# Performance work log

Measured on AMD Instinct MI355X. Metric: run time of the kernel, lower is better.

## Reference

```python
import jax, jax.numpy as jnp
import numpy as np

WZ, WH, WW = 2, 6, 12
N = WZ * WH * WW            # 144 tokens per window
DIM, HEADS = 384, 12
HD = DIM // HEADS           # 32
TOW = (8 // WZ) * (48 // WH)  # type_of_windows = 32
NW = 96 // WW               # longitude windows = 8
B_ = 1 * TOW * NW           # 256
TABLE = (2 * WW - 1) * WH * WH * WZ * WZ  # 3312


def _position_index():
    zi = np.arange(WZ); zj = -np.arange(WZ) * WZ
    hi = np.arange(WH); hj = -np.arange(WH) * WH
    w = np.arange(WW)
    c1 = np.stack(np.meshgrid(zi, hi, w, indexing='ij')).reshape(3, -1)
    c2 = np.stack(np.meshgrid(zj, hj, w, indexing='ij')).reshape(3, -1)
    coords = (c1[:, :, None] - c2[:, None, :]).transpose(1, 2, 0)  # (N, N, 3)
    coords[:, :, 2] += WW - 1
    coords[:, :, 1] *= 2 * WW - 1
    coords[:, :, 0] *= (2 * WW - 1) * WH * WH
    return coords.sum(-1).reshape(-1).astype(np.int32)  # (N*N,)


def setup_inputs() -> dict:
    key = jax.random.key(0)
    ks = jax.random.split(key, 7)
    x = jax.random.normal(ks[0], (B_, N, DIM), dtype=jnp.float32)
    mask = jax.random.normal(ks[1], (NW, N, N), dtype=jnp.float32)
    w_qkv = jax.random.normal(ks[2], (DIM, 3 * DIM), dtype=jnp.float32) * 0.02
    b_qkv = jax.random.normal(ks[3], (3 * DIM,), dtype=jnp.float32) * 0.02
    w_out = jax.random.normal(ks[4], (DIM, DIM), dtype=jnp.float32) * 0.02
    b_out = jax.random.normal(ks[5], (DIM,), dtype=jnp.float32) * 0.02
    bias_table = jax.random.normal(ks[6], (TABLE, TOW, HEADS), dtype=jnp.float32) * 0.02
    position_index = jnp.asarray(_position_index())
    return {"x": x, "mask": mask, "w_qkv": w_qkv, "b_qkv": b_qkv,
            "w_out": w_out, "b_out": b_out, "bias_table": bias_table,
            "position_index": position_index}


def reference(x, mask, w_qkv, b_qkv, w_out, b_out, bias_table, position_index):
    Bw, n, C = x.shape
    scale = HD ** -0.5
    qkv = (x @ w_qkv + b_qkv).reshape(Bw, n, 3, HEADS, HD)
    qkv = jnp.transpose(qkv, (2, 0, 3, 1, 4))  # (3, Bw, H, N, hd)
    q, k, v = qkv[0] * scale, qkv[1], qkv[2]
    attn = jnp.einsum('bhnd,bhmd->bhnm', q, k)  # (Bw, H, N, N)
    # Earth-specific bias: gather table rows by position index, tiled per window group
    r = Bw // TOW
    bias = bias_table[jnp.tile(position_index, r)]          # (r*N*N, TOW, H)
    bias = bias.reshape(n, n, -1, HEADS)                    # (N, N, Bw, H)
    bias = jnp.transpose(bias, (2, 3, 0, 1))                # (Bw, H, N, N)
    attn = attn + bias
    nW = mask.shape[0]
    attn = attn.reshape(Bw // nW, nW, HEADS, n, n) + mask[None, :, None]
    attn = jax.nn.softmax(attn.reshape(Bw, HEADS, n, n), axis=-1)
    out = jnp.einsum('bhnm,bhmd->bhnd', attn, v)            # (Bw, H, N, hd)
    out = jnp.transpose(out, (0, 2, 1, 3)).reshape(Bw, n, C)
    return out @ w_out + b_out
```

## Files before the change

### kernel.cpp

```cpp
#include <hip/hip_runtime.h>
#include <hip/hip_fp16.h>
#include <cstdint>
#include <cstddef>

#define NQQ  (144*144)
#define SCALE 0.17677669529663687f

#define AOH   0ull
#define X16H  0ull
#define QH    14155776ull
#define KH    28311552ull
#define VH    42467328ull
#define WTH   56623104ull
#define WOTH  57065472ull
#define MASKH 57212928ull
#define BIASH 57378816ull
#define WS_NEED_BYTES ((BIASH + 3072ull * 2592ull) * 2ull)

typedef _Float16 half8  __attribute__((ext_vector_type(8)));
typedef _Float16 half4v __attribute__((ext_vector_type(4)));
typedef float    f32x4  __attribute__((ext_vector_type(4)));

__launch_bounds__(256)
__global__ void k_prep(const float* __restrict__ X, _Float16* __restrict__ X16,
                       const float* __restrict__ Wq, _Float16* __restrict__ WqT,
                       const float* __restrict__ Wo, _Float16* __restrict__ WoT,
                       const float* __restrict__ M, _Float16* __restrict__ M16,
                       const float* __restrict__ table, const int* __restrict__ pidx,
                       _Float16* __restrict__ biasOut) {
    __shared__ __align__(16) char psm[13888];
    const int bid = blockIdx.x;
    const int t   = threadIdx.x;
    if (bid < 13824) {
        size_t i = (size_t)bid * 256 + t;
        float4 f = *(const float4*)&X[i * 4];
        _Float16 h[4] = {(_Float16)f.x, (_Float16)f.y, (_Float16)f.z, (_Float16)f.w};
        *(ushort4*)&X16[i * 4] = *(ushort4*)h;
        return;
    }
    if (bid >= 14130) {
        _Float16 (*sTb)[18] = (_Float16(*)[18])psm;
        int* rowsL = (int*)(psm + 13824);
        const int j      = bid - 14130;
        const int s_tile = j / 162;
        const int chunk  = j - s_tile * 162;
        const int i0     = chunk * 16;
        if (t < 16) rowsL[t] = pidx[8 * (i0 + t) + s_tile];
        __syncthreads();
#pragma unroll
        for (int rr = 0; rr < 16; ++rr) {
            int row = rowsL[rr];
            sTb[t][rr] = (_Float16)table[(size_t)row * 384 + t];
            if (t < 128) sTb[t + 256][rr] = (_Float16)table[(size_t)row * 384 + t + 256];
        }
        __syncthreads();
        unsigned int* ob = (unsigned int*)biasOut;
#pragma unroll
        for (int v = t; v < 3072; v += 256) {
            int i1h = v >> 3, dw = v & 7;
            ob[(size_t)(s_tile * 384 + i1h) * 1296 + chunk * 8 + dw] =
                *(const unsigned int*)&sTb[i1h][dw * 2];
        }
        return;
    }
    if (bid >= 13968) {
        size_t i = (size_t)(bid - 13968) * 256 + t;
        float4 f = *(const float4*)&M[i * 4];
        _Float16 h[4] = {(_Float16)f.x, (_Float16)f.y, (_Float16)f.z, (_Float16)f.w};
        *(ushort4*)&M16[i * 4] = *(ushort4*)h;
        return;
    }
    _Float16 (*sT)[72] = (_Float16(*)[72])psm;
    const float* W; _Float16* WT; int K, Cn, cb, kb;
    if (bid < 13932) {
        int j = bid - 13824;
        W = Wq; WT = WqT; K = 384; Cn = 1152;
        cb = (j % 18) * 64; kb = (j / 18) * 64;
    } else {
        int j = bid - 13932;
        W = Wo; WT = WoT; K = 384; Cn = 384;
        cb = (j % 6) * 64; kb = (j / 6) * 64;
    }
#pragma unroll
    for (int i = 0; i < 16; ++i) {
        int id = t + 256 * i;
        int kl = id >> 6, cl = id & 63;
        sT[cl][kl] = (_Float16)W[(size_t)(kb + kl) * Cn + cb + cl];
    }
    __syncthreads();
#pragma unroll
    for (int i = 0; i < 16; ++i) {
        int id = t + 256 * i;
        int cl = id >> 6, kl = id & 63;
        WT[(size_t)(cb + cl) * K + kb + kl] = sT[cl][kl];
    }
}

__launch_bounds__(256)
__global__ void k_qkv_gemm_mfma(const _Float16* __restrict__ X16,
                                const _Float16* __restrict__ WT,
                                const float* __restrict__ bq,
                                _Float16* __restrict__ ws16) {
    __shared__ _Float16 sA[128][40];
    __shared__ _Float16 sBT[128][40];
    const int t    = threadIdx.x;
    const int lane = t & 63;
    const int w    = t >> 6;
    const int quad = lane >> 4;
    const int l15  = lane & 15;
    const int r0   = blockIdx.x * 128, c0 = blockIdx.y * 128;
    const int wr   = (w >> 1) * 64, wc = (w & 1) * 64;

    f32x4 acc[4][4] = {};

    for (int kk = 0; kk < 384; kk += 32) {
#pragma unroll
        for (int i = 0; i < 2; ++i) {
            int id  = t + 256 * i;
            int row = id >> 2;
            int ko  = (id & 3) * 8;
            *(uint4*)&sA[row][ko]  = *(const uint4*)&X16[(size_t)(r0 + row) * 384 + kk + ko];
            *(uint4*)&sBT[row][ko] = *(const uint4*)&WT[(size_t)(c0 + row) * 384 + kk + ko];
        }
        __syncthreads();
        half8 a[4], b[4];
#pragma unroll
        for (int i = 0; i < 4; ++i) a[i] = *(const half8*)&sA[wr + 16 * i + l15][quad * 8];
#pragma unroll
        for (int j = 0; j < 4; ++j) b[j] = *(const half8*)&sBT[wc + 16 * j + l15][quad * 8];
#pragma unroll
        for (int i = 0; i < 4; ++i)
#pragma unroll
            for (int j = 0; j < 4; ++j)
                acc[i][j] = __builtin_amdgcn_mfma_f32_16x16x32_f16(a[i], b[j], acc[i][j], 0, 0, 0);
        __syncthreads();
    }

#pragma unroll
    for (int j = 0; j < 4; ++j) {
        int c  = c0 + wc + 16 * j + l15;
        int p  = c / 384;
        int hh = (c >> 5) % 12;
        int d0 = c & 31;
        float bias = bq[c];
        float sc   = (p == 0) ? SCALE : 1.0f;
        size_t base = (p == 0) ? QH : ((p == 1) ? KH : VH);
#pragma unroll
        for (int i = 0; i < 4; ++i) {
#pragma unroll
            for (int reg = 0; reg < 4; ++reg) {
                int r  = r0 + wr + 16 * i + quad * 4 + reg;
                int bw = r / 144;
                int n  = r - bw * 144;
                ws16[base + (((size_t)bw * 12 + hh) * 144 + n) * 32 + d0] =
                    (_Float16)((acc[i][j][reg] + bias) * sc);
            }
        }
    }
}

__launch_bounds__(576)
__global__ void k_attn_fused_mfma(const _Float16* __restrict__ ws16,
                                  const _Float16* __restrict__ mask16,
                                  const float* __restrict__ table,
                                  const int* __restrict__ pidx,
                                  const _Float16* __restrict__ bias_pre,
                                  _Float16* __restrict__ AO) {
    __shared__ __align__(16) char smem[27616];
    _Float16 (*sK)[40]   = (_Float16(*)[40])(smem);
    _Float16 (*sVT)[168] = (_Float16(*)[168])(smem + 11520);
    _Float16* sBias      = (_Float16*)(smem + 22272);

    const int bh = blockIdx.x;
    const int b  = bh / 12;
    const int h  = bh - b * 12;
    const int t  = threadIdx.x;
    const int w    = t >> 6;
    const int lane = t & 63;
    const int quad = lane >> 4;
    const int l15  = lane & 15;

    const int s_tile = b >> 5;
    const int i1     = b & 31;

    const _Float16* qg = ws16 + QH + (size_t)bh * 4608;
    const _Float16* kg = ws16 + KH + (size_t)bh * 4608;
    const _Float16* vg = ws16 + VH + (size_t)bh * 4608;

    half8 aq = *(const half8*)&qg[(size_t)(16 * w + l15) * 32 + quad * 8];

    {
        int row = t >> 2, ko = (t & 3) * 8;
        *(uint4*)&sK[row][ko] = *(const uint4*)&kg[row * 32 + ko];
    }
    for (int i = t; i < 2304; i += 576) {
        unsigned int u = ((const unsigned int*)vg)[i];
        int m  = i >> 4, d0 = (i & 15) * 2;
        int mp = m ^ ((d0 >> 3) << 3);
        sVT[d0][mp]     = ((const _Float16*)&u)[0];
        sVT[d0 + 1][mp] = ((const _Float16*)&u)[1];
    }
    if (t < 512) {
        int d = t & 31, m = 144 + (t >> 5);
        sVT[d][m ^ ((d >> 3) << 3)] = (_Float16)0;
    }
    if (bias_pre) {
        const _Float16* bg = bias_pre + (size_t)bh * 2592;
        for (int i2 = t; i2 < 648; i2 += 576) {
            uint2 wv = *(const uint2*)&bg[i2 * 4];
            int r18 = i2 / 36;
            int col = i2 * 4 - r18 * 144;
            *(uint2*)&sBias[r18 * 148 + col] = wv;
        }
    } else {
        for (int i = t; i < 2592; i += 576) {
            int row = pidx[8 * i + s_tile];
            int r18 = i / 144;
            sBias[r18 * 148 + (i - r18 * 144)] =
                (_Float16)table[(size_t)row * 384 + i1 * 12 + h];
        }
    }
    __syncthreads();

    f32x4 tj[9] = {};
#pragma unroll
    for (int j = 0; j < 9; ++j) {
        half8 bk = *(const half8*)&sK[16 * j + l15][quad * 8];
        tj[j] = __builtin_amdgcn_mfma_f32_16x16x32_f16(bk, aq, tj[j], 0, 0, 0);
    }

    const int q    = 16 * w + l15;
    const int nb18 = q % 18;
    const _Float16* mrow = mask16 + (size_t)(b & 7) * NQQ + (size_t)q * 144 + 4 * quad;
    uint2 mz[9];
#pragma unroll
    for (int j = 0; j < 9; ++j) mz[j] = *(const uint2*)&mrow[16 * j];
#pragma unroll
    for (int j = 0; j < 9; ++j) {
        uint2 bz = *(const uint2*)&sBias[nb18 * 148 + 16 * j + 4 * quad];
        const _Float16* bb = (const _Float16*)&bz;
        const _Float16* mm = (const _Float16*)&mz[j];
#pragma unroll
        for (int reg = 0; reg < 4; ++reg)
            tj[j][reg] += (float)bb[reg] + (float)mm[reg];
    }
    float rmax = tj[0][0];
#pragma unroll
    for (int j = 0; j < 9; ++j)
#pragma unroll
        for (int reg = 0; reg < 4; ++reg) rmax = fmaxf(rmax, tj[j][reg]);
    rmax = fmaxf(rmax, __shfl_xor(rmax, 16));
    rmax = fmaxf(rmax, __shfl_xor(rmax, 32));
    float rsum = 0.0f;
#pragma unroll
    for (int j = 0; j < 9; ++j)
#pragma unroll
        for (int reg = 0; reg < 4; ++reg) {
            tj[j][reg] = __expf(tj[j][reg] - rmax);
            rsum += tj[j][reg];
        }
    rsum += __shfl_xor(rsum, 16);
    rsum += __shfl_xor(rsum, 32);
    const float inv = 1.0f / rsum;

    unsigned int pkA[10], pkB[10];
    pkA[9] = 0u; pkB[9] = 0u;
#pragma unroll
    for (int j = 0; j < 9; ++j) {
        auto a2 = __builtin_amdgcn_cvt_pkrtz(tj[j][0] * inv, tj[j][1] * inv);
        auto b2 = __builtin_amdgcn_cvt_pkrtz(tj[j][2] * inv, tj[j][3] * inv);
        pkA[j] = *(unsigned int*)&a2;
        pkB[j] = *(unsigned int*)&b2;
    }

    const int src_lo = 32 * (quad & 1) + l15;
    const int src_hi = src_lo + 16;
    const bool selhi = (quad >> 1) != 0;
    f32x4 o[2] = {};
#pragma unroll
    for (int kt = 0; kt < 5; ++kt) {
        const int j0 = 2 * kt, j1 = 2 * kt + 1;
        unsigned int a0l = __shfl((int)pkA[j0], src_lo);
        unsigned int a1l = __shfl((int)pkA[j1], src_lo);
        unsigned int b0l = __shfl((int)pkB[j0], src_lo);
        unsigned int b1l = __shfl((int)pkB[j1], src_lo);
        unsigned int a0h = __shfl((int)pkA[j0], src_hi);
        unsigned int a1h = __shfl((int)pkA[j1], src_hi);
        unsigned int b0h = __shfl((int)pkB[j0], src_hi);
        unsigned int b1h = __shfl((int)pkB[j1], src_hi);
        union { uint4 u4; half8 h8; } bp;
        bp.u4.x = selhi ? a1l : a0l;
        bp.u4.y = selhi ? b1l : b0l;
        bp.u4.z = selhi ? a1h : a0h;
        bp.u4.w = selhi ? b1h : b0h;
#pragma unroll
        for (int dt = 0; dt < 2; ++dt) {
            const int vrow = dt * 16 + l15;
            half8 av = *(const half8*)&sVT[vrow][(kt * 32 + quad * 8) ^ ((vrow >> 3) << 3)];
            o[dt] = __builtin_amdgcn_mfma_f32_16x16x32_f16(av, bp.h8, o[dt], 0, 0, 0);
        }
    }

#pragma unroll
    for (int dt = 0; dt < 2; ++dt) {
        int d = dt * 16 + quad * 4;
        half4v hv;
#pragma unroll
        for (int reg = 0; reg < 4; ++reg) hv[reg] = (_Float16)o[dt][reg];
        *(half4v*)&AO[((size_t)b * 144 + q) * 384 + h * 32 + d] = hv;
    }
}

__launch_bounds__(256)
__global__ void k_out_gemm_mfma(const _Float16* __restrict__ A16,
                                const _Float16* __restrict__ WoT,
                                const float* __restrict__ bo,
                                float* __restrict__ out) {
    __shared__ _Float16 sA[128][40];
    __shared__ _Float16 sBT[128][40];
    const int t    = threadIdx.x;
    const int lane = t & 63;
    const int w    = t >> 6;
    const int quad = lane >> 4;
    const int l15  = lane & 15;
    const int r0   = blockIdx.x * 128, c0 = blockIdx.y * 128;
    const int wr   = (w >> 1) * 64, wc = (w & 1) * 64;

    f32x4 acc[4][4] = {};

    for (int kk = 0; kk < 384; kk += 32) {
#pragma unroll
        for (int i = 0; i < 2; ++i) {
            int id  = t + 256 * i;
            int row = id >> 2;
            int ko  = (id & 3) * 8;
            *(uint4*)&sA[row][ko]  = *(const uint4*)&A16[(size_t)(r0 + row) * 384 + kk + ko];
            *(uint4*)&sBT[row][ko] = *(const uint4*)&WoT[(size_t)(c0 + row) * 384 + kk + ko];
        }
        __syncthreads();
        half8 a[4], b[4];
#pragma unroll
        for (int i = 0; i < 4; ++i) a[i] = *(const half8*)&sA[wr + 16 * i + l15][quad * 8];
#pragma unroll
        for (int j = 0; j < 4; ++j) b[j] = *(const half8*)&sBT[wc + 16 * j + l15][quad * 8];
#pragma unroll
        for (int i = 0; i < 4; ++i)
#pragma unroll
            for (int j = 0; j < 4; ++j)
                acc[i][j] = __builtin_amdgcn_mfma_f32_16x16x32_f16(a[i], b[j], acc[i][j], 0, 0, 0);
        __syncthreads();
    }

#pragma unroll
    for (int j = 0; j < 4; ++j) {
        int c = c0 + wc + 16 * j + l15;
        float bias = bo[c];
#pragma unroll
        for (int i = 0; i < 4; ++i) {
#pragma unroll
            for (int reg = 0; reg < 4; ++reg) {
                int r = r0 + wr + 16 * i + quad * 4 + reg;
                out[(size_t)r * 384 + c] = acc[i][j][reg] + bias;
            }
        }
    }
}

extern "C" void kernel_launch(void* const* d_in, const int* in_sizes, int n_in,
                              void* d_out, int out_size, void* d_ws, size_t ws_size,
                              hipStream_t stream) {
    const float* x      = (const float*)d_in[0];
    const float* mask   = (const float*)d_in[1];
    const float* w_qkv  = (const float*)d_in[2];
    const float* b_qkv  = (const float*)d_in[3];
    const float* w_out  = (const float*)d_in[4];
    const float* b_out  = (const float*)d_in[5];
    const float* table  = (const float*)d_in[6];
    const int*   pidx   = (const int*)d_in[7];
    float* out = (float*)d_out;
    _Float16* ws16 = (_Float16*)d_ws;

    const bool pre = ws_size >= (size_t)WS_NEED_BYTES;
    _Float16* bias16 = pre ? (ws16 + BIASH) : (_Float16*)nullptr;

    hipLaunchKernelGGL(k_prep,          dim3(pre ? 15426 : 14130), dim3(256), 0, stream,
                       x, ws16 + X16H, w_qkv, ws16 + WTH, w_out, ws16 + WOTH,
                       mask, ws16 + MASKH, table, pidx, bias16);
    hipLaunchKernelGGL(k_qkv_gemm_mfma, dim3(288, 9), dim3(256), 0, stream,
                       ws16 + X16H, ws16 + WTH, b_qkv, ws16);
    hipLaunchKernelGGL(k_attn_fused_mfma, dim3(3072), dim3(576), 0, stream,
                       ws16, ws16 + MASKH, table, pidx, bias16, ws16 + AOH);
    hipLaunchKernelGGL(k_out_gemm_mfma, dim3(288, 3), dim3(256), 0, stream,
                       ws16 + AOH, ws16 + WOTH, b_out, out);
}
```

Measured before the change: 287.2 us.

## Use direct global-to-LDS loads, XOR swizzle and XCD-aware block remap in GEMMs

Both MFMA GEMM kernels now stage tiles with global_load_lds, which writes directly from global memory into LDS without passing through registers. The K step grows from 32 to 64, and an XOR-swizzled LDS layout is used so the half8 fragment reads avoid bank conflicts. Launches become 1D with a block-index remap that groups tiles across the 8 XCDs for better L2 locality. This roughly halves the barrier count per tile and cuts register traffic, at the cost of more LDS per block and reliance on the swizzle being consistent between the writes and the reads.

```diff
diff --git a/kernel.cpp b/kernel.cpp
--- a/kernel.cpp
+++ b/kernel.cpp
@@ -20,6 +20,10 @@
 typedef _Float16 half8  __attribute__((ext_vector_type(8)));
 typedef _Float16 half4v __attribute__((ext_vector_type(4)));
 typedef float    f32x4  __attribute__((ext_vector_type(4)));
+
+typedef __attribute__((address_space(1))) const unsigned int guint;
+typedef __attribute__((address_space(3))) unsigned int luint;
+#define GLD16(g, l) __builtin_amdgcn_global_load_lds((guint*)(g), (luint*)(l), 16, 0, 0)
 
 __launch_bounds__(256)
 __global__ void k_prep(const float* __restrict__ X, _Float16* __restrict__ X16,
@@ -101,38 +105,53 @@
                                 const _Float16* __restrict__ WT,
                                 const float* __restrict__ bq,
                                 _Float16* __restrict__ ws16) {
-    __shared__ _Float16 sA[128][40];
-    __shared__ _Float16 sBT[128][40];
+    __shared__ __align__(16) _Float16 sA[128 * 64];
+    __shared__ __align__(16) _Float16 sB[128 * 64];
     const int t    = threadIdx.x;
     const int lane = t & 63;
     const int w    = t >> 6;
     const int quad = lane >> 4;
     const int l15  = lane & 15;
-    const int r0   = blockIdx.x * 128, c0 = blockIdx.y * 128;
-    const int wr   = (w >> 1) * 64, wc = (w & 1) * 64;
+    const int bid = blockIdx.x;
+    const int wg  = (bid & 7) * 324 + (bid >> 3);
+    const int cy  = wg % 9, rx = wg / 9;
+    const int r0  = rx * 128, c0 = cy * 128;
+    const int wr  = (w >> 1) * 64, wc = (w & 1) * 64;
+
+    const int drow = t >> 3;
+    const int schk = (t & 7) ^ (drow & 7);
+    const _Float16* gA = &X16[(size_t)(r0 + drow) * 384 + schk * 8];
+    const _Float16* gB = &WT [(size_t)(c0 + drow) * 384 + schk * 8];
+    char* lA = (char*)sA + t * 16;
+    char* lB = (char*)sB + t * 16;
+
+    const int x7 = l15 & 7;
+    const char* rA = (const char*)sA + (wr + l15) * 128;
+    const char* rB = (const char*)sB + (wc + l15) * 128;
 
     f32x4 acc[4][4] = {};
 
-    for (int kk = 0; kk < 384; kk += 32) {
-#pragma unroll
-        for (int i = 0; i < 2; ++i) {
-            int id  = t + 256 * i;
-            int row = id >> 2;
-            int ko  = (id & 3) * 8;
-            *(uint4*)&sA[row][ko]  = *(const uint4*)&X16[(size_t)(r0 + row) * 384 + kk + ko];
-            *(uint4*)&sBT[row][ko] = *(const uint4*)&WT[(size_t)(c0 + row) * 384 + kk + ko];
-        }
-        __syncthreads();
-        half8 a[4], b[4];
-#pragma unroll
-        for (int i = 0; i < 4; ++i) a[i] = *(const half8*)&sA[wr + 16 * i + l15][quad * 8];
-#pragma unroll
-        for (int j = 0; j < 4; ++j) b[j] = *(const half8*)&sBT[wc + 16 * j + l15][quad * 8];
-#pragma unroll
-        for (int i = 0; i < 4; ++i)
-#pragma unroll
-            for (int j = 0; j < 4; ++j)
-                acc[i][j] = __builtin_amdgcn_mfma_f32_16x16x32_f16(a[i], b[j], acc[i][j], 0, 0, 0);
+    for (int kk = 0; kk < 384; kk += 64) {
+#pragma unroll
+        for (int j = 0; j < 4; ++j) {
+            GLD16(gA + (size_t)j * 12288 + kk, lA + j * 4096);
+            GLD16(gB + (size_t)j * 12288 + kk, lB + j * 4096);
+        }
+        __syncthreads();
+#pragma unroll
+        for (int s = 0; s < 2; ++s) {
+            const int ca = (((s * 4 + quad) ^ x7) << 4);
+            half8 a[4], b[4];
+#pragma unroll
+            for (int i = 0; i < 4; ++i) a[i] = *(const half8*)(rA + i * 2048 + ca);
+#pragma unroll
+            for (int j = 0; j < 4; ++j) b[j] = *(const half8*)(rB + j * 2048 + ca);
+#pragma unroll
+            for (int i = 0; i < 4; ++i)
+#pragma unroll
+                for (int j = 0; j < 4; ++j)
+                    acc[i][j] = __builtin_amdgcn_mfma_f32_16x16x32_f16(a[i], b[j], acc[i][j], 0, 0, 0);
+        }
         __syncthreads();
     }
 
@@ -316,38 +335,53 @@
                                 const _Float16* __restrict__ WoT,
                                 const float* __restrict__ bo,
                                 float* __restrict__ out) {
-    __shared__ _Float16 sA[128][40];
-    __shared__ _Float16 sBT[128][40];
+    __shared__ __align__(16) _Float16 sA[128 * 64];
+    __shared__ __align__(16) _Float16 sB[128 * 64];
     const int t    = threadIdx.x;
     const int lane = t & 63;
     const int w    = t >> 6;
     const int quad = lane >> 4;
     const int l15  = lane & 15;
-    const int r0   = blockIdx.x * 128, c0 = blockIdx.y * 128;
-    const int wr   = (w >> 1) * 64, wc = (w & 1) * 64;
+    const int bid = blockIdx.x;
+    const int wg  = (bid & 7) * 108 + (bid >> 3);
+    const int cy  = wg % 3, rx = wg / 3;
+    const int r0  = rx * 128, c0 = cy * 128;
+    const int wr  = (w >> 1) * 64, wc = (w & 1) * 64;
+
+    const int drow = t >> 3;
+    const int schk = (t & 7) ^ (drow & 7);
+    const _Float16* gA = &A16[(size_t)(r0 + drow) * 384 + schk * 8];
+    const _Float16* gB = &WoT[(size_t)(c0 + drow) * 384 + schk * 8];
+    char* lA = (char*)sA + t * 16;
+    char* lB = (char*)sB + t * 16;
+
+    const int x7 = l15 & 7;
+    const char* rA = (const char*)sA + (wr + l15) * 128;
+    const char* rB = (const char*)sB + (wc + l15) * 128;
 
     f32x4 acc[4][4] = {};
 
-    for (int kk = 0; kk < 384; kk += 32) {
-#pragma unroll
-        for (int i = 0; i < 2; ++i) {
-            int id  = t + 256 * i;
-            int row = id >> 2;
-            int ko  = (id & 3) * 8;
-            *(uint4*)&sA[row][ko]  = *(const uint4*)&A16[(size_t)(r0 + row) * 384 + kk + ko];
-            *(uint4*)&sBT[row][ko] = *(const uint4*)&WoT[(size_t)(c0 + row) * 384 + kk + ko];
-        }
-        __syncthreads();
-        half8 a[4], b[4];
-#pragma unroll
-        for (int i = 0; i < 4; ++i) a[i] = *(const half8*)&sA[wr + 16 * i + l15][quad * 8];
-#pragma unroll
-        for (int j = 0; j < 4; ++j) b[j] = *(const half8*)&sBT[wc + 16 * j + l15][quad * 8];
-#pragma unroll
-        for (int i = 0; i < 4; ++i)
-#pragma unroll
-            for (int j = 0; j < 4; ++j)
-                acc[i][j] = __builtin_amdgcn_mfma_f32_16x16x32_f16(a[i], b[j], acc[i][j], 0, 0, 0);
+    for (int kk = 0; kk < 384; kk += 64) {
+#pragma unroll
+        for (int j = 0; j < 4; ++j) {
+            GLD16(gA + (size_t)j * 12288 + kk, lA + j * 4096);
+            GLD16(gB + (size_t)j * 12288 + kk, lB + j * 4096);
+        }
+        __syncthreads();
+#pragma unroll
+        for (int s = 0; s < 2; ++s) {
+            const int ca = (((s * 4 + quad) ^ x7) << 4);
+            half8 a[4], b[4];
+#pragma unroll
+            for (int i = 0; i < 4; ++i) a[i] = *(const half8*)(rA + i * 2048 + ca);
+#pragma unroll
+            for (int j = 0; j < 4; ++j) b[j] = *(const half8*)(rB + j * 2048 + ca);
+#pragma unroll
+            for (int i = 0; i < 4; ++i)
+#pragma unroll
+                for (int j = 0; j < 4; ++j)
+                    acc[i][j] = __builtin_amdgcn_mfma_f32_16x16x32_f16(a[i], b[j], acc[i][j], 0, 0, 0);
+        }
         __syncthreads();
     }
 
@@ -386,10 +420,10 @@
     hipLaunchKernelGGL(k_prep,          dim3(pre ? 15426 : 14130), dim3(256), 0, stream,
                        x, ws16 + X16H, w_qkv, ws16 + WTH, w_out, ws16 + WOTH,
                        mask, ws16 + MASKH, table, pidx, bias16);
-    hipLaunchKernelGGL(k_qkv_gemm_mfma, dim3(288, 9), dim3(256), 0, stream,
+    hipLaunchKernelGGL(k_qkv_gemm_mfma, dim3(2592), dim3(256), 0, stream,
                        ws16 + X16H, ws16 + WTH, b_qkv, ws16);
     hipLaunchKernelGGL(k_attn_fused_mfma, dim3(3072), dim3(576), 0, stream,
                        ws16, ws16 + MASKH, table, pidx, bias16, ws16 + AOH);
-    hipLaunchKernelGGL(k_out_gemm_mfma, dim3(288, 3), dim3(256), 0, stream,
+    hipLaunchKernelGGL(k_out_gemm_mfma, dim3(864), dim3(256), 0, stream,
                        ws16 + AOH, ws16 + WOTH, b_out, out);
 }
```

New measurement: 257.9 us. -10.2%, faster.
